# Kernel tuning notes

Hardware: AMD Instinct MI355X
Metric: run time of the kernel (lower is better)

## Reference

```python
import jax, jax.numpy as jnp
import numpy as np

N_NODES = 100000
N_EDGES = 1600000
D_IN = 128
D_OUT = 128


def setup_inputs() -> dict:
    key = jax.random.key(0)
    k1, k2, k3, k4, k5 = jax.random.split(key, 5)
    x = jax.random.normal(k1, (N_NODES, D_IN), dtype=jnp.float32)
    edge_index = jax.random.randint(k2, (2, N_EDGES), 0, N_NODES, dtype=jnp.int64)
    # glorot-style init for params
    lin_weight = jax.random.normal(k3, (D_IN, D_OUT), dtype=jnp.float32) * (2.0 / (D_IN + D_OUT)) ** 0.5
    att_l = jax.random.normal(k4, (1, D_OUT), dtype=jnp.float32) * (2.0 / (1 + D_OUT)) ** 0.5
    att_r = jax.random.normal(k5, (1, D_OUT), dtype=jnp.float32) * (2.0 / (1 + D_OUT)) ** 0.5
    return {"x": x, "edge_index": edge_index, "lin_weight": lin_weight,
            "att_l": att_l, "att_r": att_r}


def reference(x, edge_index, lin_weight, att_l, att_r):
    # cfg: agg='add', normalize_adj=True, att=True, msg='identity',
    # combine='add', add_self_loop=False, eval mode (no dropout).
    N = x.shape[0]
    E = edge_index.shape[1]
    x = x @ lin_weight  # [N, D_OUT]
    row = edge_index[0]  # source (j)
    col = edge_index[1]  # target (i) = aggregation index

    # symmetric normalization: deg^{-1/2}[row] * w * deg^{-1/2}[col], w = 1
    edge_weight = jnp.ones((E,), dtype=x.dtype)
    deg = jax.ops.segment_sum(edge_weight, row, num_segments=N)
    deg_inv_sqrt = jnp.where(deg > 0, jax.lax.rsqrt(deg), 0.0)
    norm = deg_inv_sqrt[row] * edge_weight * deg_inv_sqrt[col]  # [E]

    # attention logits per node, gathered per edge
    alpha_l = jnp.sum(x * att_l, axis=-1)  # [N]
    alpha_r = jnp.sum(x * att_r, axis=-1)  # [N]
    a = jax.nn.relu(alpha_l[row] + alpha_r[col])  # [E]

    # segment softmax over destination node (col)
    a_max = jax.ops.segment_max(a, col, num_segments=N)
    a_exp = jnp.exp(a - a_max[col])
    a_sum = jax.ops.segment_sum(a_exp, col, num_segments=N)
    alpha = a_exp / a_sum[col]  # [E]

    # message = norm * alpha * x_j; scatter-add to targets
    msg = (norm * alpha)[:, None] * x[row]  # [E, D_OUT]
    out = jax.ops.segment_sum(msg, col, num_segments=N)  # [N, D_OUT]

    # combine='add'
    return out + x
```

## Files before the change

### kernel.cpp

```cpp
#include <hip/hip_runtime.h>
#include <cstdint>
#include <cstddef>

#define D 128
#define CAP 64
#define HB 32768
#define HS 64

typedef unsigned int uint;
typedef unsigned char uchar;
typedef __attribute__((ext_vector_type(8))) short short8;
typedef __attribute__((ext_vector_type(4))) float f32x4;
typedef __attribute__((ext_vector_type(2))) float f32x2;

__device__ inline uint pack_bf16(float a, float b) {
    uint ua = __float_as_uint(a); ua = (ua + 0x7fffu + ((ua >> 16) & 1u)) >> 16;
    uint ub = __float_as_uint(b); ub = (ub + 0x7fffu + ((ub >> 16) & 1u)) >> 16;
    return ua | (ub << 16);
}
__device__ inline short bf16_1(float a) {
    uint ua = __float_as_uint(a); ua = (ua + 0x7fffu + ((ua >> 16) & 1u)) >> 16;
    return (short)ua;
}
__device__ inline float bf16_lo(uint v) { return __uint_as_float(v << 16); }
__device__ inline float bf16_hi(uint v) { return __uint_as_float(v & 0xffff0000u); }


__global__ __launch_bounds__(256) void hist_gemm_kernel(
    const int* __restrict__ ei, uchar* __restrict__ rowpart, uchar* __restrict__ colpart,
    int E, int HBLK, int total,
    const float* __restrict__ x, const float* __restrict__ W,
    const float* __restrict__ attl, const float* __restrict__ attr,
    uint* __restrict__ xwb, uint* __restrict__ xw8,
    float* __restrict__ al_out, float* __restrict__ ar_out,
    int N)
{
    __shared__ uint smem[HB / 2];
    const int bid = blockIdx.x;
    const int tid = threadIdx.x;

    const int h_before = (int)(((long long)bid * HBLK) / total);
    const int h_incl   = (int)(((long long)(bid + 1) * HBLK) / total);

    if (h_incl > h_before) {
        const int hb = h_before;
        const int RHS_ = HBLK >> 1;
        const bool isrow = hb < RHS_;
        const int lb = isrow ? hb : hb - RHS_;
        const int g = lb / HS, s = lb % HS;
        const int c0 = g * HB;
        const int* idx = isrow ? ei : ei + E;
        uchar* partial = isrow ? rowpart : colpart;
        uint* h = smem;

        for (int i = tid; i < HB / 2; i += 256) h[i] = 0;
        __syncthreads();

        const int4* v4 = (const int4*)idx;
        const int e4 = E >> 2;
        const int chunk = (e4 + HS - 1) / HS;
        const int i0 = s * chunk;
        const int i1 = (i0 + chunk < e4) ? i0 + chunk : e4;
        for (int i = i0 + tid; i < i1; i += 256) {
            int4 v = v4[i];
            uint u;
            u = (uint)(v.x - c0); if (u < HB) atomicAdd(&h[u >> 1], (u & 1) ? 0x10000u : 1u);
            u = (uint)(v.y - c0); if (u < HB) atomicAdd(&h[u >> 1], (u & 1) ? 0x10000u : 1u);
            u = (uint)(v.z - c0); if (u < HB) atomicAdd(&h[u >> 1], (u & 1) ? 0x10000u : 1u);
            u = (uint)(v.w - c0); if (u < HB) atomicAdd(&h[u >> 1], (u & 1) ? 0x10000u : 1u);
        }
        if (s == 0) {
            for (int i = (E & ~3) + tid; i < E; i += 256) {
                uint u = (uint)(idx[i] - c0);
                if (u < HB) atomicAdd(&h[u >> 1], (u & 1) ? 0x10000u : 1u);
            }
        }
        __syncthreads();
        uint* dst = (uint*)(partial + (size_t)lb * HB);
        for (int i = tid; i < HB / 4; i += 256) {
            uint w0 = h[2 * i], w1 = h[2 * i + 1];
            uint b0 = w0 & 0xffffu; if (b0 > 255u) b0 = 255u;
            uint b1 = w0 >> 16;     if (b1 > 255u) b1 = 255u;
            uint b2 = w1 & 0xffffu; if (b2 > 255u) b2 = 255u;
            uint b3 = w1 >> 16;     if (b3 > 255u) b3 = 255u;
            dst[i] = b0 | (b1 << 8) | (b2 << 16) | (b3 << 24);
        }
        return;
    }

    short* sWt = (short*)smem;
    const int gb = bid - h_before;
    const int lane = tid & 63;
    const int w = tid >> 6;

    for (int i = tid; i < 128 * 32; i += 256) {
        int k = i >> 5, c = (i & 31) * 4;
        float4 v = ((const float4*)W)[i];
        sWt[(c + 0) * 128 + (k ^ (((c + 0) & 7) << 3))] = bf16_1(v.x);
        sWt[(c + 1) * 128 + (k ^ (((c + 1) & 7) << 3))] = bf16_1(v.y);
        sWt[(c + 2) * 128 + (k ^ (((c + 2) & 7) << 3))] = bf16_1(v.z);
        sWt[(c + 3) * 128 + (k ^ (((c + 3) & 7) << 3))] = bf16_1(v.w);
    }
    __syncthreads();

    const int colq = lane & 15;
    const int kg = lane >> 4;

    float al8[8], ar8[8];
#pragma unroll
    for (int cn = 0; cn < 8; ++cn) {
        al8[cn] = attl[cn * 16 + colq];
        ar8[cn] = attr[cn * 16 + colq];
    }

    const int rbase = gb * 128 + w * 32;

#pragma unroll
    for (int mt = 0; mt < 2; ++mt) {
        const int r0 = rbase + mt * 16;
        int rA = r0 + colq; if (rA >= N) rA = N - 1;
        const float* xp = x + (size_t)rA * D + kg * 8;

        short8 afr[4];
#pragma unroll
        for (int kt = 0; kt < 4; ++kt) {
            float4 v0 = *(const float4*)(xp + kt * 32);
            float4 v1 = *(const float4*)(xp + kt * 32 + 4);
            union { uint4 u; short8 s; } cv;
            cv.u.x = pack_bf16(v0.x, v0.y);
            cv.u.y = pack_bf16(v0.z, v0.w);
            cv.u.z = pack_bf16(v1.x, v1.y);
            cv.u.w = pack_bf16(v1.z, v1.w);
            afr[kt] = cv.s;
        }

        f32x4 acc[8];
#pragma unroll
        for (int cn = 0; cn < 8; ++cn) acc[cn] = (f32x4){0.f, 0.f, 0.f, 0.f};

#pragma unroll
        for (int cn = 0; cn < 8; ++cn) {
            const int c = cn * 16 + colq;
            const int swz = (c & 7) << 3;
#pragma unroll
            for (int kt = 0; kt < 4; ++kt) {
                short8 bfr = *(const short8*)&sWt[c * 128 + ((kt * 32 + kg * 8) ^ swz)];
                acc[cn] = __builtin_amdgcn_mfma_f32_16x16x32_bf16(afr[kt], bfr, acc[cn], 0, 0, 0);
            }
        }

#pragma unroll
        for (int j = 0; j < 4; ++j) {
            int rC = r0 + kg * 4 + j;
            float pl = 0.f, pr = 0.f;
#pragma unroll
            for (int cn = 0; cn < 8; ++cn) {
                float dv = acc[cn][j];
                pl = fmaf(dv, al8[cn], pl);
                pr = fmaf(dv, ar8[cn], pr);
                float d1v = __shfl_xor(dv, 1, 64);
                float d2v = __shfl_xor(dv, 2, 64);
                float d3v = __shfl_xor(dv, 3, 64);
                if (rC < N) {
                    if ((lane & 1) == 0)
                        xwb[(size_t)rC * 64 + cn * 8 + (colq >> 1)] = pack_bf16(dv, d1v);
                    if ((lane & 3) == 0) {
                        uint u8 = (uint)__builtin_amdgcn_cvt_pk_fp8_f32(dv, d1v, 0, false);
                        u8 = (uint)__builtin_amdgcn_cvt_pk_fp8_f32(d2v, d3v, (int)u8, true);
                        xw8[(size_t)rC * 32 + cn * 4 + (colq >> 2)] = u8;
                    }
                }
            }
#pragma unroll
            for (int o = 1; o <= 8; o <<= 1) {
                pl += __shfl_xor(pl, o, 64);
                pr += __shfl_xor(pr, o, 64);
            }
            if (colq == 0 && rC < N) { al_out[rC] = pl; ar_out[rC] = pr; }
        }
    }
}

__global__ __launch_bounds__(256) void degscan_kernel(const uchar* __restrict__ rowpart,
                                                      uchar* __restrict__ colpart,
                                                      const float* __restrict__ al,
                                                      float2* __restrict__ nd,
                                                      int* __restrict__ cnt,
                                                      int N, int NB)
{
    const int t = blockIdx.x * 256 + threadIdx.x;
    if (t >= NB) return;
    int g = t >> 15, b = t & (HB - 1);
    size_t base = (size_t)g * HS * HB + b;
    const uchar* rp = rowpart + base;
    int sum = 0;
#pragma unroll
    for (int s = 0; s < HS; ++s) sum += rp[(size_t)s * HB];
    uchar* cp = colpart + base;
    int run = 0;
    for (int s = 0; s < HS; ++s) {
        size_t ix = (size_t)s * HB;
        int v = cp[ix];
        cp[ix] = (uchar)run;
        run += v;
    }
    if (t < N) {
        float d = (float)sum;
        nd[t] = make_float2((d > 0.f) ? rsqrtf(d) : 0.f, al[t]);
        cnt[t] = run < CAP ? run : CAP;
    }
}

__global__ __launch_bounds__(1024) void scatter_kernel(const int* __restrict__ ei,
                                                       const uchar* __restrict__ colpart,
                                                       int* __restrict__ bucket, int E, int N)
{
    __shared__ int cur[HB];
    const int g = blockIdx.x / HS, s = blockIdx.x % HS, tid = threadIdx.x;
    const int c0 = g * HB;
    const uchar* sp = colpart + ((size_t)g * HS + s) * HB;
    for (int i = tid; i < HB; i += 1024)
        cur[i] = ((c0 + i) << 6) + sp[i];
    __syncthreads();
    const int4* c4 = (const int4*)(ei + E);
    const int4* r4 = (const int4*)ei;
    const int e4 = E >> 2;
    const int chunk = (e4 + HS - 1) / HS;
    const int i0 = s * chunk;
    const int i1 = (i0 + chunk < e4) ? i0 + chunk : e4;
    for (int i = i0 + tid; i < i1; i += 1024) {
        int4 c = c4[i];
        int4 r = r4[i];
        uint u; int p;
        u = (uint)(c.x - c0); if (u < HB) { p = atomicAdd(&cur[u], 1); if (p < (int)(((c0 + u) + 1) << 6)) bucket[p] = r.x; }
        u = (uint)(c.y - c0); if (u < HB) { p = atomicAdd(&cur[u], 1); if (p < (int)(((c0 + u) + 1) << 6)) bucket[p] = r.y; }
        u = (uint)(c.z - c0); if (u < HB) { p = atomicAdd(&cur[u], 1); if (p < (int)(((c0 + u) + 1) << 6)) bucket[p] = r.z; }
        u = (uint)(c.w - c0); if (u < HB) { p = atomicAdd(&cur[u], 1); if (p < (int)(((c0 + u) + 1) << 6)) bucket[p] = r.w; }
    }
    if (s == 0) {
        for (int i = (E & ~3) + tid; i < E; i += 1024) {
            uint u = (uint)(ei[E + i] - c0);
            if (u < HB) {
                int p = atomicAdd(&cur[u], 1);
                if (p < (int)(((c0 + u) + 1) << 6)) bucket[p] = ei[i];
            }
        }
    }
}

__global__ __launch_bounds__(256) void aggregate_kernel(
    const int* __restrict__ bucket,
    const int* __restrict__ cnt_arr, const float2* __restrict__ nd,
    const float* __restrict__ alpha_r, const uint* __restrict__ xwb,
    const uint* __restrict__ xw8,
    float* __restrict__ out, int N)
{
    int node = blockIdx.x * 8 + (threadIdx.x >> 5);
    int lane = threadIdx.x & 31;
    if (node >= N) return;

    int cnt = cnt_arr[node];
    int start = node << 6;
    float ar_c = alpha_r[node];
    float2 dn = nd[node];

    int r0 = 0, r1 = 0;
    float2 da0 = make_float2(0.f, 0.f), da1 = make_float2(0.f, 0.f);
    if (lane < cnt)      { r0 = bucket[start + lane];      da0 = nd[r0]; }
    if (lane + 32 < cnt) { r1 = bucket[start + lane + 32]; da1 = nd[r1]; }
    float a0 = (lane < cnt)      ? fmaxf(da0.y + ar_c, 0.f) : -1.f;
    float a1 = (lane + 32 < cnt) ? fmaxf(da1.y + ar_c, 0.f) : -1.f;

    float am = fmaxf(a0, a1);
#pragma unroll
    for (int o = 16; o >= 1; o >>= 1) am = fmaxf(am, __shfl_xor(am, o, 32));
    float p0 = (lane < cnt)      ? __expf(a0 - am) : 0.f;
    float p1 = (lane + 32 < cnt) ? __expf(a1 - am) : 0.f;
    float Sp = p0 + p1;
#pragma unroll
    for (int o = 16; o >= 1; o >>= 1) Sp += __shfl_xor(Sp, o, 32);
    float w0 = p0 * da0.x, w1 = p1 * da1.x;

    float ax = 0.f, ay = 0.f, az = 0.f, aw = 0.f;
    const int c1 = cnt < 32 ? cnt : 32;
    int k = 0;
    for (; k + 3 < c1; k += 4) {
#pragma unroll
        for (int j = 0; j < 4; ++j) {
            int rk = __shfl(r0, k + j, 32);
            float wk = __shfl(w0, k + j, 32);
            uint v = xw8[(size_t)rk * 32 + lane];
            f32x2 lo = __builtin_amdgcn_cvt_pk_f32_fp8((int)v, false);
            f32x2 hi = __builtin_amdgcn_cvt_pk_f32_fp8((int)v, true);
            ax = fmaf(wk, lo.x, ax);
            ay = fmaf(wk, lo.y, ay);
            az = fmaf(wk, hi.x, az);
            aw = fmaf(wk, hi.y, aw);
        }
    }
    for (; k < c1; ++k) {
        int rk = __shfl(r0, k, 32);
        float wk = __shfl(w0, k, 32);
        uint v = xw8[(size_t)rk * 32 + lane];
        f32x2 lo = __builtin_amdgcn_cvt_pk_f32_fp8((int)v, false);
        f32x2 hi = __builtin_amdgcn_cvt_pk_f32_fp8((int)v, true);
        ax = fmaf(wk, lo.x, ax);
        ay = fmaf(wk, lo.y, ay);
        az = fmaf(wk, hi.x, az);
        aw = fmaf(wk, hi.y, aw);
    }
    for (k = 32; k < cnt; ++k) {
        int rk = __shfl(r1, k - 32, 32);
        float wk = __shfl(w1, k - 32, 32);
        uint v = xw8[(size_t)rk * 32 + lane];
        f32x2 lo = __builtin_amdgcn_cvt_pk_f32_fp8((int)v, false);
        f32x2 hi = __builtin_amdgcn_cvt_pk_f32_fp8((int)v, true);
        ax = fmaf(wk, lo.x, ax);
        ay = fmaf(wk, lo.y, ay);
        az = fmaf(wk, hi.x, az);
        aw = fmaf(wk, hi.y, aw);
    }

    float scale = (cnt > 0) ? dn.x / Sp : 0.f;
    uint2 vc = ((const uint2*)(xwb + (size_t)node * 64))[lane];
    float4 o;
    o.x = fmaf(ax, scale, bf16_lo(vc.x));
    o.y = fmaf(ay, scale, bf16_hi(vc.x));
    o.z = fmaf(az, scale, bf16_lo(vc.y));
    o.w = fmaf(aw, scale, bf16_hi(vc.y));
    ((float4*)(out + (size_t)node * D))[lane] = o;
}

extern "C" void kernel_launch(void* const* d_in, const int* in_sizes, int n_in,
                              void* d_out, int out_size, void* d_ws, size_t ws_size,
                              hipStream_t stream)
{
    const float* x    = (const float*)d_in[0];
    const int* ei     = (const int*)d_in[1];
    const float* W    = (const float*)d_in[2];
    const float* attl = (const float*)d_in[3];
    const float* attr = (const float*)d_in[4];
    float* out = (float*)d_out;

    const int N = in_sizes[0] / D;
    const int E = in_sizes[1] / 2;
    const int ranges = (N + HB - 1) / HB;
    const int NB = ranges * HB;
    const int nb2 = NB / 256;
    const int RHS = ranges * HS;
    const int HBLK = 2 * RHS;
    const int GB = (N + 127) / 128;
    const int total = HBLK + GB;

    uint*   xwb     = (uint*)d_ws;
    uint*   xw8     = xwb + (size_t)N * 64;
    float2* nd      = (float2*)(xw8 + (size_t)N * 32);
    float*  al      = (float*)(nd + N);
    float*  ar      = al + N;
    int*    cnt     = (int*)(ar + N);
    int*    bucket  = cnt + N;
    uchar*  colpart = (uchar*)(bucket + (size_t)N * CAP);
    uchar*  rowpart = (uchar*)bucket;

    hist_gemm_kernel<<<total, 256, 0, stream>>>(ei, rowpart, colpart, E, HBLK, total,
                                                x, W, attl, attr, xwb, xw8, al, ar, N);
    degscan_kernel<<<nb2, 256, 0, stream>>>(rowpart, colpart, al, nd, cnt, N, NB);
    scatter_kernel<<<RHS, 1024, 0, stream>>>(ei, colpart, bucket, E, N);
    aggregate_kernel<<<(N + 7) / 8, 256, 0, stream>>>(bucket, cnt, nd, ar, xwb, xw8, out, N);
}
```

Baseline: 134.8 us.

## Split fused histogram/GEMM kernel into separate histogram and MFMA GEMM launches

```diff
diff --git a/kernel.cpp b/kernel.cpp
--- a/kernel.cpp
+++ b/kernel.cpp
@@ -26,70 +26,62 @@
 __device__ inline float bf16_hi(uint v) { return __uint_as_float(v & 0xffff0000u); }
 
 
-__global__ __launch_bounds__(256) void hist_gemm_kernel(
-    const int* __restrict__ ei, uchar* __restrict__ rowpart, uchar* __restrict__ colpart,
-    int E, int HBLK, int total,
+__global__ __launch_bounds__(256) void hist_both_kernel(const int* __restrict__ ei,
+                                                        uchar* __restrict__ rowpart,
+                                                        uchar* __restrict__ colpart,
+                                                        int E, int RHS)
+{
+    __shared__ uint h[HB / 2];
+    const bool isrow = (int)blockIdx.x < RHS;
+    const int lb = isrow ? blockIdx.x : blockIdx.x - RHS;
+    const int g = lb / HS, s = lb % HS, tid = threadIdx.x;
+    const int c0 = g * HB;
+    const int* idx = isrow ? ei : ei + E;
+    uchar* partial = isrow ? rowpart : colpart;
+
+    for (int i = tid; i < HB / 2; i += 256) h[i] = 0;
+    __syncthreads();
+
+    const int4* v4 = (const int4*)idx;
+    const int e4 = E >> 2;
+    const int chunk = (e4 + HS - 1) / HS;
+    const int i0 = s * chunk;
+    const int i1 = (i0 + chunk < e4) ? i0 + chunk : e4;
+    for (int i = i0 + tid; i < i1; i += 256) {
+        int4 v = v4[i];
+        uint u;
+        u = (uint)(v.x - c0); if (u < HB) atomicAdd(&h[u >> 1], (u & 1) ? 0x10000u : 1u);
+        u = (uint)(v.y - c0); if (u < HB) atomicAdd(&h[u >> 1], (u & 1) ? 0x10000u : 1u);
+        u = (uint)(v.z - c0); if (u < HB) atomicAdd(&h[u >> 1], (u & 1) ? 0x10000u : 1u);
+        u = (uint)(v.w - c0); if (u < HB) atomicAdd(&h[u >> 1], (u & 1) ? 0x10000u : 1u);
+    }
+    if (s == 0) {
+        for (int i = (E & ~3) + tid; i < E; i += 256) {
+            uint u = (uint)(idx[i] - c0);
+            if (u < HB) atomicAdd(&h[u >> 1], (u & 1) ? 0x10000u : 1u);
+        }
+    }
+    __syncthreads();
+    uint* dst = (uint*)(partial + (size_t)lb * HB);
+    for (int i = tid; i < HB / 4; i += 256) {
+        uint w0 = h[2 * i], w1 = h[2 * i + 1];
+        uint b0 = w0 & 0xffffu; if (b0 > 255u) b0 = 255u;
+        uint b1 = w0 >> 16;     if (b1 > 255u) b1 = 255u;
+        uint b2 = w1 & 0xffffu; if (b2 > 255u) b2 = 255u;
+        uint b3 = w1 >> 16;     if (b3 > 255u) b3 = 255u;
+        dst[i] = b0 | (b1 << 8) | (b2 << 16) | (b3 << 24);
+    }
+}
+
+__global__ __launch_bounds__(256) void gemm_mfma_kernel(
     const float* __restrict__ x, const float* __restrict__ W,
     const float* __restrict__ attl, const float* __restrict__ attr,
     uint* __restrict__ xwb, uint* __restrict__ xw8,
     float* __restrict__ al_out, float* __restrict__ ar_out,
     int N)
 {
-    __shared__ uint smem[HB / 2];
-    const int bid = blockIdx.x;
+    __shared__ short sWt[128 * 128];
     const int tid = threadIdx.x;
-
-    const int h_before = (int)(((long long)bid * HBLK) / total);
-    const int h_incl   = (int)(((long long)(bid + 1) * HBLK) / total);
-
-    if (h_incl > h_before) {
-        const int hb = h_before;
-        const int RHS_ = HBLK >> 1;
-        const bool isrow = hb < RHS_;
-        const int lb = isrow ? hb : hb - RHS_;
-        const int g = lb / HS, s = lb % HS;
-        const int c0 = g * HB;
-        const int* idx = isrow ? ei : ei + E;
-        uchar* partial = isrow ? rowpart : colpart;
-        uint* h = smem;
-
-        for (int i = tid; i < HB / 2; i += 256) h[i] = 0;
-        __syncthreads();
-
-        const int4* v4 = (const int4*)idx;
-        const int e4 = E >> 2;
-        const int chunk = (e4 + HS - 1) / HS;
-        const int i0 = s * chunk;
-        const int i1 = (i0 + chunk < e4) ? i0 + chunk : e4;
-        for (int i = i0 + tid; i < i1; i += 256) {
-            int4 v = v4[i];
-            uint u;
-            u = (uint)(v.x - c0); if (u < HB) atomicAdd(&h[u >> 1], (u & 1) ? 0x10000u : 1u);
-            u = (uint)(v.y - c0); if (u < HB) atomicAdd(&h[u >> 1], (u & 1) ? 0x10000u : 1u);
-            u = (uint)(v.z - c0); if (u < HB) atomicAdd(&h[u >> 1], (u & 1) ? 0x10000u : 1u);
-            u = (uint)(v.w - c0); if (u < HB) atomicAdd(&h[u >> 1], (u & 1) ? 0x10000u : 1u);
-        }
-        if (s == 0) {
-            for (int i = (E & ~3) + tid; i < E; i += 256) {
-                uint u = (uint)(idx[i] - c0);
-                if (u < HB) atomicAdd(&h[u >> 1], (u & 1) ? 0x10000u : 1u);
-            }
-        }
-        __syncthreads();
-        uint* dst = (uint*)(partial + (size_t)lb * HB);
-        for (int i = tid; i < HB / 4; i += 256) {
-            uint w0 = h[2 * i], w1 = h[2 * i + 1];
-            uint b0 = w0 & 0xffffu; if (b0 > 255u) b0 = 255u;
-            uint b1 = w0 >> 16;     if (b1 > 255u) b1 = 255u;
-            uint b2 = w1 & 0xffffu; if (b2 > 255u) b2 = 255u;
-            uint b3 = w1 >> 16;     if (b3 > 255u) b3 = 255u;
-            dst[i] = b0 | (b1 << 8) | (b2 << 16) | (b3 << 24);
-        }
-        return;
-    }
-
-    short* sWt = (short*)smem;
-    const int gb = bid - h_before;
     const int lane = tid & 63;
     const int w = tid >> 6;
 
@@ -113,7 +105,7 @@
         ar8[cn] = attr[cn * 16 + colq];
     }
 
-    const int rbase = gb * 128 + w * 32;
+    const int rbase = blockIdx.x * 128 + w * 32;
 
 #pragma unroll
     for (int mt = 0; mt < 2; ++mt) {
@@ -348,9 +340,6 @@
     const int NB = ranges * HB;
     const int nb2 = NB / 256;
     const int RHS = ranges * HS;
-    const int HBLK = 2 * RHS;
-    const int GB = (N + 127) / 128;
-    const int total = HBLK + GB;
 
     uint*   xwb     = (uint*)d_ws;
     uint*   xw8     = xwb + (size_t)N * 64;
@@ -362,8 +351,8 @@
     uchar*  colpart = (uchar*)(bucket + (size_t)N * CAP);
     uchar*  rowpart = (uchar*)bucket;
 
-    hist_gemm_kernel<<<total, 256, 0, stream>>>(ei, rowpart, colpart, E, HBLK, total,
-                                                x, W, attl, attr, xwb, xw8, al, ar, N);
+    hist_both_kernel<<<2 * RHS, 256, 0, stream>>>(ei, rowpart, colpart, E, RHS);
+    gemm_mfma_kernel<<<(N + 127) / 128, 256, 0, stream>>>(x, W, attl, attr, xwb, xw8, al, ar, N);
     degscan_kernel<<<nb2, 256, 0, stream>>>(rowpart, colpart, al, nd, cnt, N, NB);
     scatter_kernel<<<RHS, 1024, 0, stream>>>(ei, colpart, bucket, E, N);
     aggregate_kernel<<<(N + 7) / 8, 256, 0, stream>>>(bucket, cnt, nd, ar, xwb, xw8, out, N);
```

New measurement: 133.6 us. About the same (-0.9%).
